# Optimization experiments

Hardware: AMD Instinct MI355X
Metric: run time of the kernel (lower is better)

## Reference

```python
import jax, jax.numpy as jnp
import numpy as np

PATCH = 4      # patch_size
WIN = 8        # win_size (== win_stride, non-overlapping windows)
TAU = 0.05     # sinkhorn_tau
ITERS = 20     # sinkhorn_iters
EPS = 1e-6


def setup_inputs() -> dict:
    key = jax.random.key(0)
    k0, k1 = jax.random.split(key)
    B, C, H, W = 16, 4, 256, 256
    z0 = jax.random.normal(k0, (B, C, H, W), jnp.float32)
    z1 = jax.random.normal(k1, (B, C, H, W), jnp.float32)
    return {"z0": z0, "z1": z1}


def _token_feats(z):
    # patchify_latents + L2 normalize (F.normalize eps clamp). groupmean proj
    # is identity since d_match == token_dim.
    B, C, H, W = z.shape
    hp, wp = H // PATCH, W // PATCH
    t = z.reshape(B, C, hp, PATCH, wp, PATCH).transpose(0, 2, 4, 1, 3, 5)
    t = t.reshape(B, hp, wp, C * PATCH * PATCH)          # (B,hp,wp,D)
    n = jnp.maximum(jnp.sqrt(jnp.sum(t * t, axis=-1, keepdims=True)), EPS)
    return t / n


def _to_windows(f):
    B, hp, wp, D = f.shape
    nh, nw = hp // WIN, wp // WIN
    w = f.reshape(B, nh, WIN, nw, WIN, D).transpose(0, 1, 3, 2, 4, 5)
    return w.reshape(B * nh * nw, WIN * WIN, D)


def _sinkhorn_log(logits):
    # _sinkhorn_log_batch: alternate row (dim 2) / col (dim 1) logsumexp
    def step(lp, _):
        lp = lp - jax.nn.logsumexp(lp, axis=2, keepdims=True)
        lp = lp - jax.nn.logsumexp(lp, axis=1, keepdims=True)
        return lp, None
    lp, _ = jax.lax.scan(step, logits, None, length=ITERS)
    return lp


def _grid_sample_border(img, gx, gy):
    # F.grid_sample bilinear, padding_mode='border', align_corners=True,
    # with gx/gy already in absolute pixel coords (B,H,W).
    B, C, H, W = img.shape
    gx = jnp.clip(gx, 0.0, W - 1.0)
    gy = jnp.clip(gy, 0.0, H - 1.0)
    x0f = jnp.floor(gx); y0f = jnp.floor(gy)
    wx = (gx - x0f)[:, None]; wy = (gy - y0f)[:, None]   # (B,1,H,W)
    x0 = jnp.clip(x0f.astype(jnp.int32), 0, W - 1)
    x1 = jnp.clip(x0 + 1, 0, W - 1)
    y0 = jnp.clip(y0f.astype(jnp.int32), 0, H - 1)
    y1 = jnp.clip(y0 + 1, 0, H - 1)
    flat = img.reshape(B, C, H * W)

    def gat(yi, xi):
        idx = (yi * W + xi).reshape(B, 1, H * W)
        idx = jnp.broadcast_to(idx, (B, C, H * W))
        return jnp.take_along_axis(flat, idx, axis=2).reshape(B, C, H, W)

    v00 = gat(y0, x0); v01 = gat(y0, x1)
    v10 = gat(y1, x0); v11 = gat(y1, x1)
    return (v00 * (1 - wx) * (1 - wy) + v01 * wx * (1 - wy)
            + v10 * (1 - wx) * wy + v11 * wx * wy)


def reference(z0, z1):
    B, C, H, W = z0.shape
    hp, wp = H // PATCH, W // PATCH
    nh, nw = hp // WIN, wp // WIN
    f0 = _token_feats(z0)
    f1 = _token_feats(z1)
    w0 = _to_windows(f0)                                  # (BW, M, D)
    w1 = _to_windows(f1)
    logits = jnp.einsum('wid,wjd->wij', w0, w1) / TAU     # (BW, M, M)
    logp = _sinkhorn_log(logits)
    Pm = jax.nn.softmax(logp, axis=-1)                    # row-normalized plan
    # expected target position per source token (local window coords, x/y)
    ys, xs = jnp.meshgrid(jnp.arange(WIN), jnp.arange(WIN), indexing='ij')
    pos = jnp.stack([xs.ravel(), ys.ravel()], axis=-1).astype(z0.dtype)  # (M,2)
    disp = Pm @ pos - pos                                 # (BW, M, 2) token units
    disp = disp.reshape(B, nh, nw, WIN, WIN, 2).transpose(0, 1, 3, 2, 4, 5)
    disp = disp.reshape(B, hp, wp, 2)
    # token flow -> pixel flow (nearest upsample, scale by patch size)
    flow = jnp.repeat(jnp.repeat(disp, PATCH, axis=1), PATCH, axis=2) * PATCH
    yy, xx = jnp.meshgrid(jnp.arange(H, dtype=z0.dtype),
                          jnp.arange(W, dtype=z0.dtype), indexing='ij')
    gx = xx[None] + flow[..., 0]
    gy = yy[None] + flow[..., 1]
    return _grid_sample_border(z1, gx, gy)
```

## Files before the change

kernel.cpp:

```cpp
#include <hip/hip_runtime.h>
#include <math.h>


#define S0 68

__device__ __forceinline__ float rlane(float v, int l) {
    return __uint_as_float(__builtin_amdgcn_readlane(__float_as_uint(v), l));
}

__global__ __launch_bounds__(256, 3)
void skw_kernel(const float* __restrict__ z0, const float* __restrict__ z1,
                float* __restrict__ out) {
    __shared__ float f0[64 * S0];
    __shared__ float f1[64 * S0];
    __shared__ float psq0[256], psq1[256];
    __shared__ float invn0[64], invn1[64];
    __shared__ float dispx[64], dispy[64];

    const int t   = threadIdx.x;
    const int blk = blockIdx.x;
    const int b   = blk >> 6;
    const int wy  = (blk >> 3) & 7;
    const int wx  = blk & 7;
    const int Y0  = wy * 32, X0 = wx * 32;

    const int xq = t & 7;
    const int yy = (t >> 3) & 31;
    const int mm = (yy >> 2) * 8 + xq;
    const int pi = yy & 3;

    {
        const size_t base = (size_t)(b * 4) * 65536 + (size_t)(Y0 + yy) * 256 + X0 + xq * 4;
        const float* s0p = z0 + base;
        const float* s1p = z1 + base;
        float a0 = 0.f, a1 = 0.f;
        #pragma unroll
        for (int c = 0; c < 4; ++c) {
            float4 v0 = *(const float4*)(s0p + c * 65536);
            float4 v1 = *(const float4*)(s1p + c * 65536);
            a0 += v0.x*v0.x + v0.y*v0.y + v0.z*v0.z + v0.w*v0.w;
            a1 += v1.x*v1.x + v1.y*v1.y + v1.z*v1.z + v1.w*v1.w;
            *(float4*)&f0[mm * S0 + c * 16 + pi * 4] = v0;
            *(float4*)&f1[mm * S0 + c * 16 + pi * 4] = v1;
        }
        psq0[t] = a0; psq1[t] = a1;
    }
    __syncthreads();
    if (t < 128) {
        const int u2 = t & 63;
        const float* ps = (t < 64) ? psq0 : psq1;
        const int ti = u2 >> 3, tj = u2 & 7;
        float s = ps[(ti*4+0)*8+tj] + ps[(ti*4+1)*8+tj]
                + ps[(ti*4+2)*8+tj] + ps[(ti*4+3)*8+tj];
        float r = 1.0f / fmaxf(sqrtf(s), 1e-6f);
        if (t < 64) invn0[u2] = r; else invn1[u2] = r;
    }
    __syncthreads();

    const int bi = t >> 4, bj = t & 15;
    float acc[4][4];
    #pragma unroll
    for (int r = 0; r < 4; ++r)
        #pragma unroll
        for (int s2 = 0; s2 < 4; ++s2) acc[r][s2] = 0.f;

    #pragma unroll 4
    for (int dc = 0; dc < 16; ++dc) {
        float4 A[4], Bv[4];
        #pragma unroll
        for (int r = 0; r < 4; ++r)  A[r]  = *(const float4*)&f0[(bi*4+r)*S0 + dc*4];
        #pragma unroll
        for (int s2 = 0; s2 < 4; ++s2) Bv[s2] = *(const float4*)&f1[(bj*4+s2)*S0 + dc*4];
        #pragma unroll
        for (int r = 0; r < 4; ++r)
            #pragma unroll
            for (int s2 = 0; s2 < 4; ++s2)
                acc[r][s2] += A[r].x*Bv[s2].x + A[r].y*Bv[s2].y
                            + A[r].z*Bv[s2].z + A[r].w*Bv[s2].w;
    }
    float si[4], sj[4];
    #pragma unroll
    for (int r = 0; r < 4; ++r)  si[r] = invn0[bi*4+r] * 20.0f;
    #pragma unroll
    for (int s2 = 0; s2 < 4; ++s2) sj[s2] = invn1[bj*4+s2];
    __syncthreads();
    float* Mm = f0;
    #pragma unroll
    for (int r = 0; r < 4; ++r) {
        float4 o;
        o.x = acc[r][0]*si[r]*sj[0];
        o.y = acc[r][1]*si[r]*sj[1];
        o.z = acc[r][2]*si[r]*sj[2];
        o.w = acc[r][3]*si[r]*sj[3];
        *(float4*)&Mm[(bi*4+r)*S0 + bj*4] = o;
    }
    __syncthreads();

    const int lane = t & 63;
    if ((t >> 6) == (blk & 3)) {
        float K[64], KT[64];
        #pragma unroll
        for (int j4 = 0; j4 < 16; ++j4) {
            float4 r4 = *(const float4*)&Mm[lane * S0 + j4 * 4];
            K[4*j4+0] = __expf(r4.x); K[4*j4+1] = __expf(r4.y);
            K[4*j4+2] = __expf(r4.z); K[4*j4+3] = __expf(r4.w);
        }
        #pragma unroll
        for (int j = 0; j < 64; ++j) KT[j] = __expf(Mm[j * S0 + lane]);

        float u, v;
        {
            float s0=0.f, s1=0.f, s2=0.f, s3=0.f;
            #pragma unroll
            for (int j = 0; j < 64; j += 4) {
                s0 += K[j]; s1 += K[j+1]; s2 += K[j+2]; s3 += K[j+3];
            }
            u = 1.0f / ((s0+s1) + (s2+s3));
        }
        #pragma unroll 1
        for (int it = 0; it < 19; ++it) {
            float s0=0.f, s1=0.f, s2=0.f, s3=0.f;
            #pragma unroll
            for (int j = 0; j < 64; j += 4) {
                s0 = fmaf(KT[j  ], rlane(u, j  ), s0);
                s1 = fmaf(KT[j+1], rlane(u, j+1), s1);
                s2 = fmaf(KT[j+2], rlane(u, j+2), s2);
                s3 = fmaf(KT[j+3], rlane(u, j+3), s3);
            }
            v = 1.0f / ((s0+s1) + (s2+s3));
            s0=0.f; s1=0.f; s2=0.f; s3=0.f;
            #pragma unroll
            for (int j = 0; j < 64; j += 4) {
                s0 = fmaf(K[j  ], rlane(v, j  ), s0);
                s1 = fmaf(K[j+1], rlane(v, j+1), s1);
                s2 = fmaf(K[j+2], rlane(v, j+2), s2);
                s3 = fmaf(K[j+3], rlane(v, j+3), s3);
            }
            u = 1.0f / ((s0+s1) + (s2+s3));
        }
        {
            float s0=0.f, s1=0.f, s2=0.f, s3=0.f;
            #pragma unroll
            for (int j = 0; j < 64; j += 4) {
                s0 = fmaf(KT[j  ], rlane(u, j  ), s0);
                s1 = fmaf(KT[j+1], rlane(u, j+1), s1);
                s2 = fmaf(KT[j+2], rlane(u, j+2), s2);
                s3 = fmaf(KT[j+3], rlane(u, j+3), s3);
            }
            v = 1.0f / ((s0+s1) + (s2+s3));
        }
        {
            float ss=0.f, sx=0.f, sy=0.f;
            #pragma unroll
            for (int j = 0; j < 64; ++j) {
                float pj = K[j] * rlane(v, j);
                ss += pj;
                sx = fmaf(pj, (float)(j & 7),  sx);
                sy = fmaf(pj, (float)(j >> 3), sy);
            }
            const float inv = 1.0f / ss;
            dispx[lane] = sx * inv - (float)(lane & 7);
            dispy[lane] = sy * inv - (float)(lane >> 3);
        }
    }
    __syncthreads();

    #pragma unroll
    for (int rep = 0; rep < 4; ++rep) {
        const int p = rep * 256 + t;
        const int y = p >> 5, x = p & 31;
        const int m2 = (y >> 2) * 8 + (x >> 2);
        float gx = (float)(X0 + x) + 4.0f * dispx[m2];
        float gy = (float)(Y0 + y) + 4.0f * dispy[m2];
        gx = fminf(fmaxf(gx, 0.0f), 255.0f);
        gy = fminf(fmaxf(gy, 0.0f), 255.0f);
        const float x0f = floorf(gx), y0f = floorf(gy);
        const float wxf = gx - x0f, wyf = gy - y0f;
        const int xi0 = (int)x0f, yi0 = (int)y0f;
        const int xi1 = min(xi0 + 1, 255), yi1 = min(yi0 + 1, 255);
        const float w00 = (1.f-wxf)*(1.f-wyf), w01 = wxf*(1.f-wyf);
        const float w10 = (1.f-wxf)*wyf,       w11 = wxf*wyf;
        const float* basep = z1 + (size_t)(b * 4) * 65536;
        #pragma unroll
        for (int c = 0; c < 4; ++c) {
            const float* pc = basep + c * 65536;
            const float v00 = pc[yi0*256 + xi0], v01 = pc[yi0*256 + xi1];
            const float v10 = pc[yi1*256 + xi0], v11 = pc[yi1*256 + xi1];
            out[((size_t)(b*4+c)*256 + (Y0+y))*256 + X0 + x]
                = v00*w00 + v01*w01 + v10*w10 + v11*w11;
        }
    }
}

extern "C" void kernel_launch(void* const* d_in, const int* in_sizes, int n_in,
                              void* d_out, int out_size, void* d_ws, size_t ws_size,
                              hipStream_t stream) {
    (void)in_sizes; (void)n_in; (void)d_ws; (void)ws_size; (void)out_size;
    const float* z0 = (const float*)d_in[0];
    const float* z1 = (const float*)d_in[1];
    float* out = (float*)d_out;
    skw_kernel<<<dim3(1024), dim3(256), 0, stream>>>(z0, z1, out);
}
```

Before: 119.0 us.

## Drop KT register array, read column sums from LDS, transpose f1 for GEMM

Computes exp once per element during the GEMM writeback and stores K in LDS. The Sinkhorn column pass now reads K columns straight from shared memory instead of holding a 64-float transposed copy in registers. This frees registers so the launch bound can rise from 3 to 4 blocks per CU. f1 is stored transposed so the GEMM reads contiguous float4 along the token axis. The trade-off is 64 extra LDS reads per column pass in each of 20 iterations, which lengthens the serial single-wave Sinkhorn loop, plus scalar transposed LDS stores that may bank-conflict.

```diff
diff --git a/kernel.cpp b/kernel.cpp
--- a/kernel.cpp
+++ b/kernel.cpp
@@ -8,11 +8,11 @@
     return __uint_as_float(__builtin_amdgcn_readlane(__float_as_uint(v), l));
 }
 
-__global__ __launch_bounds__(256, 3)
+__global__ __launch_bounds__(256, 4)
 void skw_kernel(const float* __restrict__ z0, const float* __restrict__ z1,
                 float* __restrict__ out) {
-    __shared__ float f0[64 * S0];
-    __shared__ float f1[64 * S0];
+    __shared__ float f0 [64 * S0];
+    __shared__ float f1t[64 * S0];
     __shared__ float psq0[256], psq1[256];
     __shared__ float invn0[64], invn1[64];
     __shared__ float dispx[64], dispy[64];
@@ -33,17 +33,26 @@
         const size_t base = (size_t)(b * 4) * 65536 + (size_t)(Y0 + yy) * 256 + X0 + xq * 4;
         const float* s0p = z0 + base;
         const float* s1p = z1 + base;
-        float a0 = 0.f, a1 = 0.f;
+        float a0 = 0.f;
         #pragma unroll
         for (int c = 0; c < 4; ++c) {
-            float4 v0 = *(const float4*)(s0p + c * 65536);
-            float4 v1 = *(const float4*)(s1p + c * 65536);
-            a0 += v0.x*v0.x + v0.y*v0.y + v0.z*v0.z + v0.w*v0.w;
-            a1 += v1.x*v1.x + v1.y*v1.y + v1.z*v1.z + v1.w*v1.w;
-            *(float4*)&f0[mm * S0 + c * 16 + pi * 4] = v0;
-            *(float4*)&f1[mm * S0 + c * 16 + pi * 4] = v1;
-        }
-        psq0[t] = a0; psq1[t] = a1;
+            float4 vv = *(const float4*)(s0p + c * 65536);
+            a0 += vv.x*vv.x + vv.y*vv.y + vv.z*vv.z + vv.w*vv.w;
+            *(float4*)&f0[mm * S0 + c * 16 + pi * 4] = vv;
+        }
+        psq0[t] = a0;
+        float a1 = 0.f;
+        #pragma unroll
+        for (int c = 0; c < 4; ++c) {
+            float4 vv = *(const float4*)(s1p + c * 65536);
+            a1 += vv.x*vv.x + vv.y*vv.y + vv.z*vv.z + vv.w*vv.w;
+            const int d = c * 16 + pi * 4;
+            f1t[(d+0)*S0 + mm] = vv.x;
+            f1t[(d+1)*S0 + mm] = vv.y;
+            f1t[(d+2)*S0 + mm] = vv.z;
+            f1t[(d+3)*S0 + mm] = vv.w;
+        }
+        psq1[t] = a1;
     }
     __syncthreads();
     if (t < 128) {
@@ -68,15 +77,16 @@
     for (int dc = 0; dc < 16; ++dc) {
         float4 A[4], Bv[4];
         #pragma unroll
-        for (int r = 0; r < 4; ++r)  A[r]  = *(const float4*)&f0[(bi*4+r)*S0 + dc*4];
-        #pragma unroll
-        for (int s2 = 0; s2 < 4; ++s2) Bv[s2] = *(const float4*)&f1[(bj*4+s2)*S0 + dc*4];
-        #pragma unroll
-        for (int r = 0; r < 4; ++r)
-            #pragma unroll
-            for (int s2 = 0; s2 < 4; ++s2)
-                acc[r][s2] += A[r].x*Bv[s2].x + A[r].y*Bv[s2].y
-                            + A[r].z*Bv[s2].z + A[r].w*Bv[s2].w;
+        for (int r = 0; r < 4; ++r) A[r] = *(const float4*)&f0[(bi*4+r)*S0 + dc*4];
+        #pragma unroll
+        for (int dd = 0; dd < 4; ++dd) Bv[dd] = *(const float4*)&f1t[(dc*4+dd)*S0 + bj*4];
+        #pragma unroll
+        for (int r = 0; r < 4; ++r) {
+            acc[r][0] += A[r].x*Bv[0].x + A[r].y*Bv[1].x + A[r].z*Bv[2].x + A[r].w*Bv[3].x;
+            acc[r][1] += A[r].x*Bv[0].y + A[r].y*Bv[1].y + A[r].z*Bv[2].y + A[r].w*Bv[3].y;
+            acc[r][2] += A[r].x*Bv[0].z + A[r].y*Bv[1].z + A[r].z*Bv[2].z + A[r].w*Bv[3].z;
+            acc[r][3] += A[r].x*Bv[0].w + A[r].y*Bv[1].w + A[r].z*Bv[2].w + A[r].w*Bv[3].w;
+        }
     }
     float si[4], sj[4];
     #pragma unroll
@@ -88,26 +98,23 @@
     #pragma unroll
     for (int r = 0; r < 4; ++r) {
         float4 o;
-        o.x = acc[r][0]*si[r]*sj[0];
-        o.y = acc[r][1]*si[r]*sj[1];
-        o.z = acc[r][2]*si[r]*sj[2];
-        o.w = acc[r][3]*si[r]*sj[3];
+        o.x = __expf(acc[r][0]*si[r]*sj[0]);
+        o.y = __expf(acc[r][1]*si[r]*sj[1]);
+        o.z = __expf(acc[r][2]*si[r]*sj[2]);
+        o.w = __expf(acc[r][3]*si[r]*sj[3]);
         *(float4*)&Mm[(bi*4+r)*S0 + bj*4] = o;
     }
     __syncthreads();
 
     const int lane = t & 63;
     if ((t >> 6) == (blk & 3)) {
-        float K[64], KT[64];
+        float K[64];
         #pragma unroll
         for (int j4 = 0; j4 < 16; ++j4) {
             float4 r4 = *(const float4*)&Mm[lane * S0 + j4 * 4];
-            K[4*j4+0] = __expf(r4.x); K[4*j4+1] = __expf(r4.y);
-            K[4*j4+2] = __expf(r4.z); K[4*j4+3] = __expf(r4.w);
-        }
-        #pragma unroll
-        for (int j = 0; j < 64; ++j) KT[j] = __expf(Mm[j * S0 + lane]);
-
+            K[4*j4+0] = r4.x; K[4*j4+1] = r4.y;
+            K[4*j4+2] = r4.z; K[4*j4+3] = r4.w;
+        }
         float u, v;
         {
             float s0=0.f, s1=0.f, s2=0.f, s3=0.f;
@@ -121,11 +128,11 @@
         for (int it = 0; it < 19; ++it) {
             float s0=0.f, s1=0.f, s2=0.f, s3=0.f;
             #pragma unroll
-            for (int j = 0; j < 64; j += 4) {
-                s0 = fmaf(KT[j  ], rlane(u, j  ), s0);
-                s1 = fmaf(KT[j+1], rlane(u, j+1), s1);
-                s2 = fmaf(KT[j+2], rlane(u, j+2), s2);
-                s3 = fmaf(KT[j+3], rlane(u, j+3), s3);
+            for (int i = 0; i < 64; i += 4) {
+                s0 = fmaf(Mm[(i+0)*S0 + lane], rlane(u, i+0), s0);
+                s1 = fmaf(Mm[(i+1)*S0 + lane], rlane(u, i+1), s1);
+                s2 = fmaf(Mm[(i+2)*S0 + lane], rlane(u, i+2), s2);
+                s3 = fmaf(Mm[(i+3)*S0 + lane], rlane(u, i+3), s3);
             }
             v = 1.0f / ((s0+s1) + (s2+s3));
             s0=0.f; s1=0.f; s2=0.f; s3=0.f;
@@ -141,11 +148,11 @@
         {
             float s0=0.f, s1=0.f, s2=0.f, s3=0.f;
             #pragma unroll
-            for (int j = 0; j < 64; j += 4) {
-                s0 = fmaf(KT[j  ], rlane(u, j  ), s0);
-                s1 = fmaf(KT[j+1], rlane(u, j+1), s1);
-                s2 = fmaf(KT[j+2], rlane(u, j+2), s2);
-                s3 = fmaf(KT[j+3], rlane(u, j+3), s3);
+            for (int i = 0; i < 64; i += 4) {
+                s0 = fmaf(Mm[(i+0)*S0 + lane], rlane(u, i+0), s0);
+                s1 = fmaf(Mm[(i+1)*S0 + lane], rlane(u, i+1), s1);
+                s2 = fmaf(Mm[(i+2)*S0 + lane], rlane(u, i+2), s2);
+                s3 = fmaf(Mm[(i+3)*S0 + lane], rlane(u, i+3), s3);
             }
             v = 1.0f / ((s0+s1) + (s2+s3));
         }
```

Result: slower. 122.9 us (+3.3%).
